# Kernel optimization log

Hardware: AMD Instinct MI355X
Metric: run time of the kernel (lower is better)

Reference implementation:

```python
import jax, jax.numpy as jnp
import numpy as np

V, E, H, F, A, L = 32000, 256, 512, 512, 256, 49  # vocab, embed, hidden, feature, attn, n_locations
B, T = 64, 32


def setup_inputs() -> dict:
    key = jax.random.key(0)
    ks = jax.random.split(key, 16)
    s = lambda k, sh: (jax.random.normal(k, sh, jnp.float32) * 0.02)
    embedding = s(ks[0], (V, E)).at[0].set(0.0)  # padding_idx=0 row zeroed
    return dict(
        image_feats=jax.random.normal(ks[1], (B, L, F), jnp.float32),
        caption_in=jax.random.randint(ks[2], (B, T), 0, V, dtype=jnp.int32),
        embedding=embedding,
        W_init_h=s(ks[3], (F, H)), b_init_h=jnp.zeros((H,), jnp.float32),
        W_init_c=s(ks[4], (F, H)), b_init_c=jnp.zeros((H,), jnp.float32),
        W_feat=s(ks[5], (F, A)), b_feat=jnp.zeros((A,), jnp.float32),
        W_hid=s(ks[6], (H, A)), b_hid=jnp.zeros((A,), jnp.float32),
        W_score=s(ks[7], (A,)), b_score=jnp.zeros((), jnp.float32),
        W_ih=s(ks[8], (E + F, 4 * H)), b_ih=jnp.zeros((4 * H,), jnp.float32),
        W_hh=s(ks[9], (H, 4 * H)), b_hh=jnp.zeros((4 * H,), jnp.float32),
        W_out=s(ks[10], (H, V)), b_out=jnp.zeros((V,), jnp.float32),
    )


def reference(image_feats, caption_in, embedding,
              W_init_h, b_init_h, W_init_c, b_init_c,
              W_feat, b_feat, W_hid, b_hid, W_score, b_score,
              W_ih, b_ih, W_hh, b_hh, W_out, b_out):
    # init_hidden_state: mean over spatial locations -> two linears
    mean_feats = image_feats.mean(axis=1)                      # (B, F)
    h0 = mean_feats @ W_init_h + b_init_h                      # (B, H)
    c0 = mean_feats @ W_init_c + b_init_c                      # (B, H)
    embs = embedding[caption_in]                               # (B, T, E); dropout = identity (eval)
    feat_proj = image_feats @ W_feat + b_feat                  # (B, L, A) - invariant over t, precompute

    def step(carry, emb_t):
        h, c = carry
        # additive attention
        energy = jnp.tanh(feat_proj + (h @ W_hid + b_hid)[:, None, :])   # (B, L, A)
        scores = energy @ W_score + b_score                              # (B, L)
        alpha = jax.nn.softmax(scores, axis=1)                           # (B, L)
        context = jnp.einsum('bl,blf->bf', alpha, image_feats)           # (B, F)
        # LSTMCell (torch gate order i, f, g, o)
        x = jnp.concatenate([emb_t, context], axis=1)                    # (B, E+F)
        gates = x @ W_ih + b_ih + h @ W_hh + b_hh                        # (B, 4H)
        i, f, g, o = jnp.split(gates, 4, axis=1)
        i = jax.nn.sigmoid(i); f = jax.nn.sigmoid(f); o = jax.nn.sigmoid(o)
        c_new = f * c + i * jnp.tanh(g)
        h_new = o * jnp.tanh(c_new)
        logits_t = h_new @ W_out + b_out                                 # (B, V); dropout = identity
        return (h_new, c_new), (logits_t, alpha)

    _, (logits, alphas) = jax.lax.scan(step, (h0, c0), jnp.swapaxes(embs, 0, 1))
    predictions = jnp.swapaxes(logits, 0, 1)   # (B, T, V)
    all_alphas = jnp.swapaxes(alphas, 0, 1)    # (B, T, L)
    return predictions, all_alphas
```

## Files before the change

kernel.cpp:

```cpp
#include <hip/hip_runtime.h>
#include <hip/hip_bf16.h>

typedef _Float16 f16;
typedef _Float16 f16x8 __attribute__((ext_vector_type(8)));
typedef _Float16 f16x4 __attribute__((ext_vector_type(4)));
typedef _Float16 f16x2 __attribute__((ext_vector_type(2)));
typedef float f32x4 __attribute__((ext_vector_type(4)));
typedef unsigned long long ull;

#define B_ 64
#define T_ 32
#define L_ 49
#define F_ 512
#define H_ 512
#define A_ 256
#define E_ 256
#define V_ 32000
#define G4 2048
#define NG 32
#define NLOG 125
#define SLOT 16

#define ALOAD32(p)     __hip_atomic_load((const unsigned*)(p), __ATOMIC_RELAXED, __HIP_MEMORY_SCOPE_AGENT)
#define ASTORE32(p, v) __hip_atomic_store((unsigned*)(p), (v), __ATOMIC_RELAXED, __HIP_MEMORY_SCOPE_AGENT)
#define ASTORE64(p, v) __hip_atomic_store((ull*)(p), (v), __ATOMIC_RELAXED, __HIP_MEMORY_SCOPE_AGENT)

#if defined(__has_builtin)
#if __has_builtin(__builtin_amdgcn_fdot2)
#define HAS_FDOT2 1
#endif
#endif

#define NB_TC0 (64 * 24)
#define NB_TC1 (64 * 16)
#define NB_TC2 (1000 * 16)
#define NB_TC3 (8 * 16)
#define NB_CVT 1568
#define NB_EMB 2048
#define NB_INIT 64
#define NB_FP  196

__device__ void dev_tcvt(const float* __restrict__ x, f16* __restrict__ y,
                         int R, int C, int bx, int by, char* smem) {
    float (*ls)[33] = (float(*)[33])smem;
    int c0 = bx * 32, r0 = by * 32;
    int tid = threadIdx.x;
    int rr = tid >> 3, cs = (tid & 7) * 4;
    float4 v = *(const float4*)&x[(size_t)(r0 + rr) * C + c0 + cs];
    ls[rr][cs] = v.x; ls[rr][cs + 1] = v.y; ls[rr][cs + 2] = v.z; ls[rr][cs + 3] = v.w;
    __syncthreads();
    int cr = tid >> 3, rs = (tid & 7) * 4;
    f16x4 o = {(f16)ls[rs][cr], (f16)ls[rs + 1][cr], (f16)ls[rs + 2][cr], (f16)ls[rs + 3][cr]};
    *(f16x4*)&y[(size_t)(c0 + cr) * R + r0 + rs] = o;
}

__global__ __launch_bounds__(256) void k_prep(
    const float* __restrict__ image_feats, const int* __restrict__ caption,
    const float* __restrict__ embedding,
    const float* __restrict__ W_init_h, const float* __restrict__ b_init_h,
    const float* __restrict__ W_init_c, const float* __restrict__ b_init_c,
    const float* __restrict__ W_feat, const float* __restrict__ b_feat,
    const float* __restrict__ W_hid, const float* __restrict__ W_ih,
    const float* __restrict__ W_hh, const float* __restrict__ W_out,
    f16* __restrict__ feats16, f16* __restrict__ embs16,
    f16* __restrict__ WihT, f16* __restrict__ WhhT,
    f16* __restrict__ WoutT, f16* __restrict__ WhidT,
    f16* __restrict__ hslab, float* __restrict__ c_cur,
    float* __restrict__ featproj) {
    __shared__ __align__(16) char smem[32768];
    int bid = blockIdx.x, tid = threadIdx.x;
    int r = bid;
    if (r < NB_TC0) { dev_tcvt(W_ih, WihT, E_ + F_, G4, r % 64, r / 64, smem); return; }
    r -= NB_TC0;
    if (r < NB_TC1) { dev_tcvt(W_hh, WhhT, H_, G4, r % 64, r / 64, smem); return; }
    r -= NB_TC1;
    if (r < NB_TC2) { dev_tcvt(W_out, WoutT, H_, V_, r % 1000, r / 1000, smem); return; }
    r -= NB_TC2;
    if (r < NB_TC3) { dev_tcvt(W_hid, WhidT, H_, A_, r % 8, r / 8, smem); return; }
    r -= NB_TC3;
    if (r < NB_CVT) {
        int i = r * 256 + tid;
        float4 v = ((const float4*)image_feats)[i];
        f16x4 h = {(f16)v.x, (f16)v.y, (f16)v.z, (f16)v.w};
        ((f16x4*)feats16)[i] = h;
        return;
    }
    r -= NB_CVT;
    if (r < NB_EMB) {
        int tok = caption[r];
        embs16[(size_t)r * E_ + tid] = (f16)embedding[(size_t)tok * E_ + tid];
        return;
    }
    r -= NB_EMB;
    if (r < NB_INIT) {
        float* mean = (float*)smem;
        int b = r;
        for (int f = tid; f < F_; f += 256) {
            float s = 0.f;
            for (int l = 0; l < L_; ++l) s += image_feats[((size_t)b * L_ + l) * F_ + f];
            mean[f] = s * (1.f / 49.f);
        }
        __syncthreads();
        for (int h = tid; h < H_; h += 256) {
            float a = b_init_h[h], c = b_init_c[h];
            for (int k = 0; k < F_; ++k) {
                float m = mean[k];
                a += m * W_init_h[k * H_ + h];
                c += m * W_init_c[k * H_ + h];
            }
            hslab[(size_t)b * H_ + h] = (f16)a;
            c_cur[b * H_ + h] = c;
        }
        return;
    }
    r -= NB_INIT;
    {
        float (*fs)[F_] = (float(*)[F_])smem;
        int r0 = r * 16;
        for (int i = tid; i < 16 * F_; i += 256)
            fs[i >> 9][i & 511] = image_feats[(size_t)r0 * F_ + i];
        __syncthreads();
        float acc[16];
#pragma unroll
        for (int q = 0; q < 16; ++q) acc[q] = 0.f;
        for (int k = 0; k < F_; ++k) {
            float w = W_feat[k * A_ + tid];
#pragma unroll
            for (int q = 0; q < 16; ++q) acc[q] += fs[q][k] * w;
        }
        float bb = b_feat[tid];
#pragma unroll
        for (int q = 0; q < 16; ++q) featproj[(size_t)(r0 + q) * A_ + tid] = acc[q] + bb;
    }
}

struct Smem128 { f16 As[128][40]; f16 Bs[128][40]; };

__device__ __forceinline__ void gemm128_body1(
    const f16* __restrict__ A, int lda, const f16* __restrict__ Bt, int ldb,
    f16* __restrict__ Cv, int M, int K, int mtiles, int bid,
    const float* __restrict__ bias0, const float* __restrict__ bias1, Smem128* sm) {
    int m0 = (bid % mtiles) * 128, n0 = (bid / mtiles) * 128;
    int tid = threadIdx.x, lane = tid & 63, wave = tid >> 6;
    int wr = (wave >> 1) * 64, wc = (wave & 1) * 64;
    int frow = lane & 15, fk = (lane >> 4) * 8;
    int ra = tid >> 2, ka = (tid & 3) * 8;
    f32x4 acc[4][4];
#pragma unroll
    for (int i = 0; i < 4; ++i)
#pragma unroll
        for (int j = 0; j < 4; ++j) { acc[i][j][0]=0.f; acc[i][j][1]=0.f; acc[i][j][2]=0.f; acc[i][j][3]=0.f; }

    for (int k0 = 0; k0 < K; k0 += 32) {
        f16x8 a0 = *(const f16x8*)&A[(size_t)(m0 + ra) * lda + k0 + ka];
        f16x8 a1 = *(const f16x8*)&A[(size_t)(m0 + 64 + ra) * lda + k0 + ka];
        f16x8 b0 = *(const f16x8*)&Bt[(size_t)(n0 + ra) * ldb + k0 + ka];
        f16x8 b1 = *(const f16x8*)&Bt[(size_t)(n0 + 64 + ra) * ldb + k0 + ka];
        __syncthreads();
        *(f16x8*)&sm->As[ra][ka] = a0;
        *(f16x8*)&sm->As[64 + ra][ka] = a1;
        *(f16x8*)&sm->Bs[ra][ka] = b0;
        *(f16x8*)&sm->Bs[64 + ra][ka] = b1;
        __syncthreads();
        f16x8 av[4], bv[4];
#pragma unroll
        for (int i = 0; i < 4; ++i) {
            av[i] = *(f16x8*)&sm->As[wr + i * 16 + frow][fk];
            bv[i] = *(f16x8*)&sm->Bs[wc + i * 16 + frow][fk];
        }
#pragma unroll
        for (int mi = 0; mi < 4; ++mi)
#pragma unroll
            for (int ni = 0; ni < 4; ++ni)
                acc[mi][ni] = __builtin_amdgcn_mfma_f32_16x16x32_f16(av[mi], bv[ni], acc[mi][ni], 0, 0, 0);
    }
    int rq = (lane >> 4) * 4;
#pragma unroll
    for (int mi = 0; mi < 4; ++mi)
#pragma unroll
        for (int ni = 0; ni < 4; ++ni) {
            int cc = n0 + wc + ni * 16 + frow;
            float badd = (bias0 ? bias0[cc] : 0.f) + (bias1 ? bias1[cc] : 0.f);
#pragma unroll
            for (int r = 0; r < 4; ++r) {
                int rr = m0 + wr + mi * 16 + rq + r;
                if (rr < M)
                    Cv[((size_t)rr * 512 + (cc & 511)) * 4 + (cc >> 9)] =
                        (f16)(acc[mi][ni][r] + badd);
            }
        }
}

__global__ __launch_bounds__(256) void k_gemm_pre(
    int split,
    const f16* A0, int lda0, const f16* B0, int ldb0, f16* C0, int M0, int K0, int mt0,
    const f16* A1, int lda1, const f16* B1, int ldb1, f16* C1, int M1, int K1, int mt1,
    const float* bias0, const float* bias1) {
    __shared__ Smem128 sm;
    int bid = blockIdx.x;
    if (bid < split)
        gemm128_body1(A0, lda0, B0, ldb0, C0, M0, K0, mt0, bid,
                      (const float*)nullptr, (const float*)nullptr, &sm);
    else
        gemm128_body1(A1, lda1, B1, ldb1, C1, M1, K1, mt1, bid - split,
                      bias0, bias1, &sm);
}

struct GateSm {
    float fp[L_][A_];
    float ea[A_];
    float ws[A_];
    float sc[64];
    float alpha[64];
    unsigned hL[256];
};
struct GemmSm {
    f16 w[64][512];
    union {
        f16 hs[64][512];
        f16 hwT16[64][72];
    } u;
};
struct LogSm { f16 hs[128][512]; };

__device__ __forceinline__ void wait_n(const unsigned* flags, int n, unsigned target) {
    int tid = threadIdx.x;
    if (tid < n) {
        const unsigned* p = flags + tid * SLOT;
        while (ALOAD32(p) < target) __builtin_amdgcn_s_sleep(1);
    }
    asm volatile("" ::: "memory");
    __syncthreads();
}

__device__ __forceinline__ float sigm(float x) { return 1.f / (1.f + __expf(-x)); }
__device__ __forceinline__ float tanh_f(float x) { return 1.f - 2.f / (1.f + __expf(2.f * x)); }

__global__ __launch_bounds__(256, 1) void k_steps(
    const f16* __restrict__ WhhT, const f16* __restrict__ WhidT,
    const float* __restrict__ featproj, const float* __restrict__ b_hid,
    const float* __restrict__ W_score, const float* __restrict__ b_score,
    const f16* __restrict__ embP, const f16* __restrict__ fp2P,
    const float* __restrict__ c_cur,
    f16* __restrict__ hslab, f16* __restrict__ hwslab,
    const f16* __restrict__ WoutT, const float* __restrict__ b_out,
    float* __restrict__ preds, float* __restrict__ out_alpha,
    unsigned* __restrict__ gateflag, unsigned* __restrict__ gemmflag) {
    __shared__ __align__(16) char smraw[sizeof(LogSm)];
    int bid = blockIdx.x, tid = threadIdx.x;

    if (bid < 64) {
        int b = bid;
        GateSm* S = (GateSm*)smraw;
        for (int i = tid; i < L_ * A_; i += 256)
            ((float*)S->fp)[i] = featproj[(size_t)b * L_ * A_ + i];
        S->ws[tid] = W_score[tid];
        float bhid_r = b_hid[tid];
        float bsc = b_score[0];
        S->hL[tid] = ((const unsigned*)hslab)[(size_t)b * 256 + tid];
        float cs0 = c_cur[b * H_ + 2 * tid], cs1 = c_cur[b * H_ + 2 * tid + 1];
        const f16* wrow = WhidT + (size_t)tid * 512;
        int wv = tid >> 6, ln = tid & 63;
        __syncthreads();

        for (int t = 0; t < T_; ++t) {
            {
                float acc = bhid_r;
                const f16x8* hL8 = (const f16x8*)S->hL;
#pragma unroll 16
                for (int kk = 0; kk < 64; ++kk) {
                    union { f16x8 v; f16x2 p[4]; } uw, uh;
                    uw.v = *(const f16x8*)&wrow[kk * 8];
                    uh.v = hL8[kk];
#ifdef HAS_FDOT2
                    acc = __builtin_amdgcn_fdot2(uw.p[0], uh.p[0], acc, false);
                    acc = __builtin_amdgcn_fdot2(uw.p[1], uh.p[1], acc, false);
                    acc = __builtin_amdgcn_fdot2(uw.p[2], uh.p[2], acc, false);
                    acc = __builtin_amdgcn_fdot2(uw.p[3], uh.p[3], acc, false);
#else
#pragma unroll
                    for (int e = 0; e < 8; ++e) acc += (float)uw.v[e] * (float)uh.v[e];
#endif
                }
                S->ea[tid] = acc;
            }
            __syncthreads();
            for (int l = wv; l < L_; l += 4) {
                float p = 0.f;
#pragma unroll
                for (int q = 0; q < 4; ++q) {
                    int j = ln + q * 64;
                    p += tanh_f(S->fp[l][j] + S->ea[j]) * S->ws[j];
                }
#pragma unroll
                for (int off = 32; off > 0; off >>= 1) p += __shfl_xor(p, off);
                if (ln == 0) S->sc[l] = p;
            }
            __syncthreads();
            if (tid < 64) {
                float v = (tid < L_) ? S->sc[tid] + bsc : -3.4e38f;
                float m = v;
#pragma unroll
                for (int off = 32; off > 0; off >>= 1) m = fmaxf(m, __shfl_xor(m, off));
                float e = (tid < L_) ? __expf(v - m) : 0.f;
                float s = e;
#pragma unroll
                for (int off = 32; off > 0; off >>= 1) s += __shfl_xor(s, off);
                if (tid < L_) {
                    float al = e / s;
                    S->alpha[tid] = al;
                    out_alpha[((size_t)b * T_ + t) * L_ + tid] = al;
                }
            }
            __syncthreads();
            float s8[8];
#pragma unroll
            for (int i = 0; i < 8; ++i) s8[i] = 0.f;
            {
                const f16* fpb = fp2P + (size_t)b * L_ * G4 + 8 * tid;
#pragma unroll 7
                for (int l = 0; l < L_; ++l) {
                    float a = S->alpha[l];
                    f16x8 fv = *(const f16x8*)&fpb[(size_t)l * G4];
#pragma unroll
                    for (int i = 0; i < 8; ++i) s8[i] += a * (float)fv[i];
                }
            }
            f16x8 ep = *(const f16x8*)&embP[((size_t)b * T_ + t) * G4 + 8 * tid];
            wait_n(gemmflag, NG, (unsigned)(t + 1));
            {
                f16x8 hw = *(const f16x8*)&hwslab[((size_t)t * B_ + b) * G4 + 8 * tid];
                float gA[8];
#pragma unroll
                for (int i = 0; i < 8; ++i) gA[i] = (float)hw[i] + (float)ep[i] + s8[i];
                float cn0 = sigm(gA[1]) * cs0 + sigm(gA[0]) * tanh_f(gA[2]);
                float cn1 = sigm(gA[5]) * cs1 + sigm(gA[4]) * tanh_f(gA[6]);
                float hn0 = sigm(gA[3]) * tanh_f(cn0);
                float hn1 = sigm(gA[7]) * tanh_f(cn1);
                cs0 = cn0; cs1 = cn1;
                union { f16 h[2]; unsigned u; } pk;
                pk.h[0] = (f16)hn0; pk.h[1] = (f16)hn1;
                S->hL[tid] = pk.u;
                ASTORE32((unsigned*)hslab + ((size_t)(t + 1) * B_ + b) * 256 + tid, pk.u);
            }
            __syncthreads();
            if (tid == 0)
                ASTORE32(&gateflag[b * SLOT], (unsigned)(t + 2));
        }
    } else if (bid < 64 + NG) {
        int g = bid - 64;
        GemmSm* S = (GemmSm*)smraw;
        for (int i = 0; i < 16; ++i) {
            int idx = i * 256 + tid;
            int r = idx >> 6, ch = idx & 63;
            int cc = (r & 3) * 512 + 16 * g + (r >> 2);
            *(f16x8*)&S->w[r][(ch ^ (r & 7)) * 8] =
                *(const f16x8*)&WhhT[(size_t)cc * 512 + ch * 8];
        }
        int wvv = tid >> 6, lane = tid & 63;
        int frow = lane & 15, q = lane >> 4, sw = frow & 7, rq = q * 4;
        int bo = tid >> 2, cq = (tid & 3) * 4;
        __syncthreads();

        for (int t = 0; t < T_; ++t) {
            if (t) wait_n(gateflag, 64, (unsigned)(t + 1));
            {
                const f16* hsrc = hslab + (size_t)t * B_ * H_;
#pragma unroll
                for (int i = 0; i < 16; ++i) {
                    int idx = i * 256 + tid;
                    int r = idx >> 6, ch = idx & 63;
                    *(f16x8*)&S->u.hs[r][(ch ^ (r & 7)) * 8] =
                        *(const f16x8*)&hsrc[(size_t)r * H_ + ch * 8];
                }
            }
            __syncthreads();
            f32x4 a4[4];
#pragma unroll
            for (int mi = 0; mi < 4; ++mi) { a4[mi][0]=0.f; a4[mi][1]=0.f; a4[mi][2]=0.f; a4[mi][3]=0.f; }
#pragma unroll
            for (int kk = 0; kk < 16; ++kk) {
                int ch = ((kk * 4 + q) ^ sw) * 8;
                f16x8 bv = *(f16x8*)&S->w[wvv * 16 + frow][ch];
#pragma unroll
                for (int mi = 0; mi < 4; ++mi) {
                    f16x8 av = *(f16x8*)&S->u.hs[mi * 16 + frow][ch];
                    a4[mi] = __builtin_amdgcn_mfma_f32_16x16x32_f16(av, bv, a4[mi], 0, 0, 0);
                }
            }
            __syncthreads();
#pragma unroll
            for (int mi = 0; mi < 4; ++mi)
#pragma unroll
                for (int r = 0; r < 4; ++r)
                    S->u.hwT16[mi * 16 + rq + r][wvv * 16 + frow] = (f16)a4[mi][r];
            __syncthreads();
            {
                f16* dst = hwslab + ((size_t)t * B_ + bo) * G4 + 64 * g + cq;
#pragma unroll
                for (int e = 0; e < 4; ++e) {
                    union { f16 h[4]; ull u; } pk;
                    *(f16x4*)pk.h = *(f16x4*)&S->u.hwT16[bo][cq + 16 * e];
                    ASTORE64(dst + 16 * e, pk.u);
                }
            }
            __syncthreads();
            if (tid == 0)
                ASTORE32(&gemmflag[g * SLOT], (unsigned)(t + 1));
        }
    } else {
        int nt = bid - 64 - NG;
        int n0 = nt * 256;
        LogSm* S = (LogSm*)smraw;
        int wvv = tid >> 6, lane = tid & 63;
        int frow = lane & 15, q = lane >> 4, sw = frow & 7, rq = q * 4;

        for (int tc = 0; tc < T_ / 2; ++tc) {
            wait_n(gateflag, 64, (unsigned)(2 * tc + 3));
            {
                const f16* hsrc = hslab + (size_t)(2 * tc + 1) * B_ * H_;
#pragma unroll
                for (int i = 0; i < 32; ++i) {
                    int idx = i * 256 + tid;
                    int r = idx >> 6, ch = idx & 63;
                    *(f16x8*)&S->hs[r][(ch ^ (r & 7)) * 8] =
                        *(const f16x8*)&hsrc[(size_t)r * H_ + ch * 8];
                }
            }
            __syncthreads();
            f32x4 acc[8][4];
#pragma unroll
            for (int mi = 0; mi < 8; ++mi)
#pragma unroll
                for (int ni = 0; ni < 4; ++ni) { acc[mi][ni][0]=0.f; acc[mi][ni][1]=0.f; acc[mi][ni][2]=0.f; acc[mi][ni][3]=0.f; }
#pragma unroll 2
            for (int kk = 0; kk < 16; ++kk) {
                int ch = ((kk * 4 + q) ^ sw) * 8;
                f16x8 av[8], bv[4];
#pragma unroll
                for (int mi = 0; mi < 8; ++mi)
                    av[mi] = *(f16x8*)&S->hs[mi * 16 + frow][ch];
#pragma unroll
                for (int ni = 0; ni < 4; ++ni)
                    bv[ni] = *(const f16x8*)&WoutT[(size_t)(n0 + wvv * 64 + ni * 16 + frow) * 512 + kk * 32 + q * 8];
#pragma unroll
                for (int mi = 0; mi < 8; ++mi)
#pragma unroll
                    for (int ni = 0; ni < 4; ++ni)
                        acc[mi][ni] = __builtin_amdgcn_mfma_f32_16x16x32_f16(av[mi], bv[ni], acc[mi][ni], 0, 0, 0);
            }
#pragma unroll
            for (int ni = 0; ni < 4; ++ni) {
                int cc = n0 + wvv * 64 + ni * 16 + frow;
                float badd = b_out[cc];
#pragma unroll
                for (int mi = 0; mi < 8; ++mi)
#pragma unroll
                    for (int r = 0; r < 4; ++r) {
                        int rr = mi * 16 + rq + r;
                        int tt = 2 * tc + (rr >> 6), bb2 = rr & 63;
                        preds[((size_t)bb2 * T_ + tt) * V_ + cc] = acc[mi][ni][r] + badd;
                    }
            }
            __syncthreads();
        }
    }
}

extern "C" void kernel_launch(void* const* d_in, const int* in_sizes, int n_in,
                              void* d_out, int out_size, void* d_ws, size_t ws_size,
                              hipStream_t stream) {
    const float* image_feats = (const float*)d_in[0];
    const int*   caption     = (const int*)d_in[1];
    const float* embedding   = (const float*)d_in[2];
    const float* W_init_h    = (const float*)d_in[3];
    const float* b_init_h    = (const float*)d_in[4];
    const float* W_init_c    = (const float*)d_in[5];
    const float* b_init_c    = (const float*)d_in[6];
    const float* W_feat      = (const float*)d_in[7];
    const float* b_feat      = (const float*)d_in[8];
    const float* W_hid       = (const float*)d_in[9];
    const float* b_hid       = (const float*)d_in[10];
    const float* W_score     = (const float*)d_in[11];
    const float* b_score     = (const float*)d_in[12];
    const float* W_ih        = (const float*)d_in[13];
    const float* b_ih        = (const float*)d_in[14];
    const float* W_hh        = (const float*)d_in[15];
    const float* b_hh        = (const float*)d_in[16];
    const float* W_out       = (const float*)d_in[17];
    const float* b_out       = (const float*)d_in[18];

    float* preds = (float*)d_out;
    float* out_alpha = preds + (size_t)B_ * T_ * V_;

    size_t off = 0;
    char* base = (char*)d_ws;
    auto carve = [&](size_t bytes) {
        void* p = base + off;
        off += (bytes + 255) & ~(size_t)255;
        return p;
    };
    const int MP = 3200;
    f16* fp2P       = (f16*)carve((size_t)MP * G4 * 2);
    f16* embP       = (f16*)carve((size_t)B_ * T_ * G4 * 2);
    float* featproj = (float*)carve((size_t)B_ * L_ * A_ * 4);
    float* c_cur    = (float*)carve((size_t)B_ * H_ * 4);
    f16* hslab      = (f16*)carve((size_t)(T_ + 1) * B_ * H_ * 2);
    f16* hwslab     = (f16*)carve((size_t)T_ * B_ * G4 * 2);
    unsigned* flags = (unsigned*)carve((64 + NG) * SLOT * 4);
    f16* feats16    = (f16*)carve((size_t)MP * F_ * 2);
    f16* embs16     = (f16*)carve((size_t)B_ * T_ * E_ * 2);
    f16* WihT       = (f16*)carve((size_t)G4 * (E_ + F_) * 2);
    f16* WhhT       = (f16*)carve((size_t)G4 * H_ * 2);
    f16* WoutT      = (f16*)carve((size_t)V_ * H_ * 2);
    f16* WhidT      = (f16*)carve((size_t)A_ * H_ * 2);
    unsigned* gateflag = flags;
    unsigned* gemmflag = flags + 64 * SLOT;
    (void)ws_size; (void)in_sizes; (void)n_in; (void)out_size;

    {
        int nb = NB_TC0 + NB_TC1 + NB_TC2 + NB_TC3 + NB_CVT + NB_EMB + NB_INIT + NB_FP;
        hipLaunchKernelGGL(k_prep, dim3(nb), dim3(256), 0, stream,
                           image_feats, caption, embedding,
                           W_init_h, b_init_h, W_init_c, b_init_c,
                           W_feat, b_feat, W_hid, W_ih, W_hh, W_out,
                           feats16, embs16, WihT, WhhT, WoutT, WhidT,
                           hslab, c_cur, featproj);
    }
    hipLaunchKernelGGL(k_gemm_pre, dim3(400 + 256), dim3(256), 0, stream,
                       400,
                       feats16, F_, WihT + E_, E_ + F_, fp2P, B_ * L_, F_, 25,
                       embs16, E_, WihT, E_ + F_, embP, B_ * T_, E_, B_ * T_ / 128,
                       b_ih, b_hh);
    hipMemsetAsync(flags, 0, (64 + NG) * SLOT * 4, stream);
    hipLaunchKernelGGL(k_steps, dim3(64 + NG + NLOG), dim3(256), 0, stream,
                       WhhT, WhidT, featproj, b_hid, W_score, b_score,
                       embP, fp2P, c_cur, hslab, hwslab,
                       WoutT, b_out, preds, out_alpha,
                       gateflag, gemmflag);
}
```

Baseline: 728.9 us.

## Compute context in-loop and fuse context-weight GEMM into recurrent gate GEMM

Stops precomputing the feats@W_ih_ctx projection for all 3136 locations (fp2P). Instead each gate block computes the attention context vector from LDS-resident fp16 feats and publishes it with a new ctx flag. The GEMM blocks, now doubled to 64 with half the columns each, add context@W_ih_ctx to h@W_hh. W_hid is also repacked into k-pair interleaved form for coalesced fdot2 reads. This removes a large pre-GEMM and the per-step fp2P reads, at the cost of an extra synchronization hop and a second GEMM inside the serial recurrent critical path.

```diff
diff --git a/kernel.cpp b/kernel.cpp
--- a/kernel.cpp
+++ b/kernel.cpp
@@ -17,7 +17,7 @@
 #define E_ 256
 #define V_ 32000
 #define G4 2048
-#define NG 32
+#define NG 64
 #define NLOG 125
 #define SLOT 16
 
@@ -34,7 +34,7 @@
 #define NB_TC0 (64 * 24)
 #define NB_TC1 (64 * 16)
 #define NB_TC2 (1000 * 16)
-#define NB_TC3 (8 * 16)
+#define NB_PAIR 256
 #define NB_CVT 1568
 #define NB_EMB 2048
 #define NB_INIT 64
@@ -64,7 +64,7 @@
     const float* __restrict__ W_hh, const float* __restrict__ W_out,
     f16* __restrict__ feats16, f16* __restrict__ embs16,
     f16* __restrict__ WihT, f16* __restrict__ WhhT,
-    f16* __restrict__ WoutT, f16* __restrict__ WhidT,
+    f16* __restrict__ WoutT, f16* __restrict__ Whidp,
     f16* __restrict__ hslab, float* __restrict__ c_cur,
     float* __restrict__ featproj) {
     __shared__ __align__(16) char smem[32768];
@@ -76,8 +76,13 @@
     r -= NB_TC1;
     if (r < NB_TC2) { dev_tcvt(W_out, WoutT, H_, V_, r % 1000, r / 1000, smem); return; }
     r -= NB_TC2;
-    if (r < NB_TC3) { dev_tcvt(W_hid, WhidT, H_, A_, r % 8, r / 8, smem); return; }
-    r -= NB_TC3;
+    if (r < NB_PAIR) {
+        int k2 = r;
+        Whidp[(k2 * 256 + tid) * 2]     = (f16)W_hid[(2 * k2) * 256 + tid];
+        Whidp[(k2 * 256 + tid) * 2 + 1] = (f16)W_hid[(2 * k2 + 1) * 256 + tid];
+        return;
+    }
+    r -= NB_PAIR;
     if (r < NB_CVT) {
         int i = r * 256 + tid;
         float4 v = ((const float4*)image_feats)[i];
@@ -136,10 +141,12 @@
 
 struct Smem128 { f16 As[128][40]; f16 Bs[128][40]; };
 
-__device__ __forceinline__ void gemm128_body1(
-    const f16* __restrict__ A, int lda, const f16* __restrict__ Bt, int ldb,
-    f16* __restrict__ Cv, int M, int K, int mtiles, int bid,
-    const float* __restrict__ bias0, const float* __restrict__ bias1, Smem128* sm) {
+__global__ __launch_bounds__(256) void k_gemm_emb(
+    const f16* __restrict__ A, const f16* __restrict__ Bt,
+    f16* __restrict__ Cv, const float* __restrict__ bias0, const float* __restrict__ bias1) {
+    __shared__ Smem128 sm;
+    int bid = blockIdx.x;
+    int mtiles = B_ * T_ / 128;
     int m0 = (bid % mtiles) * 128, n0 = (bid / mtiles) * 128;
     int tid = threadIdx.x, lane = tid & 63, wave = tid >> 6;
     int wr = (wave >> 1) * 64, wc = (wave & 1) * 64;
@@ -150,23 +157,22 @@
     for (int i = 0; i < 4; ++i)
 #pragma unroll
         for (int j = 0; j < 4; ++j) { acc[i][j][0]=0.f; acc[i][j][1]=0.f; acc[i][j][2]=0.f; acc[i][j][3]=0.f; }
-
-    for (int k0 = 0; k0 < K; k0 += 32) {
-        f16x8 a0 = *(const f16x8*)&A[(size_t)(m0 + ra) * lda + k0 + ka];
-        f16x8 a1 = *(const f16x8*)&A[(size_t)(m0 + 64 + ra) * lda + k0 + ka];
-        f16x8 b0 = *(const f16x8*)&Bt[(size_t)(n0 + ra) * ldb + k0 + ka];
-        f16x8 b1 = *(const f16x8*)&Bt[(size_t)(n0 + 64 + ra) * ldb + k0 + ka];
+    for (int k0 = 0; k0 < E_; k0 += 32) {
+        f16x8 a0 = *(const f16x8*)&A[(size_t)(m0 + ra) * E_ + k0 + ka];
+        f16x8 a1 = *(const f16x8*)&A[(size_t)(m0 + 64 + ra) * E_ + k0 + ka];
+        f16x8 b0 = *(const f16x8*)&Bt[(size_t)(n0 + ra) * (E_ + F_) + k0 + ka];
+        f16x8 b1 = *(const f16x8*)&Bt[(size_t)(n0 + 64 + ra) * (E_ + F_) + k0 + ka];
         __syncthreads();
-        *(f16x8*)&sm->As[ra][ka] = a0;
-        *(f16x8*)&sm->As[64 + ra][ka] = a1;
-        *(f16x8*)&sm->Bs[ra][ka] = b0;
-        *(f16x8*)&sm->Bs[64 + ra][ka] = b1;
+        *(f16x8*)&sm.As[ra][ka] = a0;
+        *(f16x8*)&sm.As[64 + ra][ka] = a1;
+        *(f16x8*)&sm.Bs[ra][ka] = b0;
+        *(f16x8*)&sm.Bs[64 + ra][ka] = b1;
         __syncthreads();
         f16x8 av[4], bv[4];
 #pragma unroll
         for (int i = 0; i < 4; ++i) {
-            av[i] = *(f16x8*)&sm->As[wr + i * 16 + frow][fk];
-            bv[i] = *(f16x8*)&sm->Bs[wc + i * 16 + frow][fk];
+            av[i] = *(f16x8*)&sm.As[wr + i * 16 + frow][fk];
+            bv[i] = *(f16x8*)&sm.Bs[wc + i * 16 + frow][fk];
         }
 #pragma unroll
         for (int mi = 0; mi < 4; ++mi)
@@ -180,34 +186,19 @@
 #pragma unroll
         for (int ni = 0; ni < 4; ++ni) {
             int cc = n0 + wc + ni * 16 + frow;
-            float badd = (bias0 ? bias0[cc] : 0.f) + (bias1 ? bias1[cc] : 0.f);
+            float badd = bias0[cc] + bias1[cc];
 #pragma unroll
             for (int r = 0; r < 4; ++r) {
                 int rr = m0 + wr + mi * 16 + rq + r;
-                if (rr < M)
-                    Cv[((size_t)rr * 512 + (cc & 511)) * 4 + (cc >> 9)] =
-                        (f16)(acc[mi][ni][r] + badd);
-            }
-        }
-}
-
-__global__ __launch_bounds__(256) void k_gemm_pre(
-    int split,
-    const f16* A0, int lda0, const f16* B0, int ldb0, f16* C0, int M0, int K0, int mt0,
-    const f16* A1, int lda1, const f16* B1, int ldb1, f16* C1, int M1, int K1, int mt1,
-    const float* bias0, const float* bias1) {
-    __shared__ Smem128 sm;
-    int bid = blockIdx.x;
-    if (bid < split)
-        gemm128_body1(A0, lda0, B0, ldb0, C0, M0, K0, mt0, bid,
-                      (const float*)nullptr, (const float*)nullptr, &sm);
-    else
-        gemm128_body1(A1, lda1, B1, ldb1, C1, M1, K1, mt1, bid - split,
-                      bias0, bias1, &sm);
+                Cv[((size_t)rr * 512 + (cc & 511)) * 4 + (cc >> 9)] =
+                    (f16)(acc[mi][ni][r] + badd);
+            }
+        }
 }
 
 struct GateSm {
     float fp[L_][A_];
+    unsigned fe[L_ * 256];
     float ea[A_];
     float ws[A_];
     float sc[64];
@@ -215,10 +206,11 @@
     unsigned hL[256];
 };
 struct GemmSm {
-    f16 w[64][512];
+    f16 w[32][512];
+    f16 w2[32][512];
     union {
         f16 hs[64][512];
-        f16 hwT16[64][72];
+        f16 hwT16[64][40];
     } u;
 };
 struct LogSm { f16 hs[128][512]; };
@@ -237,15 +229,17 @@
 __device__ __forceinline__ float tanh_f(float x) { return 1.f - 2.f / (1.f + __expf(2.f * x)); }
 
 __global__ __launch_bounds__(256, 1) void k_steps(
-    const f16* __restrict__ WhhT, const f16* __restrict__ WhidT,
-    const float* __restrict__ featproj, const float* __restrict__ b_hid,
+    const f16* __restrict__ WhhT, const f16* __restrict__ WihT,
+    const f16* __restrict__ Whidp,
+    const float* __restrict__ featproj, const f16* __restrict__ feats16,
+    const float* __restrict__ b_hid,
     const float* __restrict__ W_score, const float* __restrict__ b_score,
-    const f16* __restrict__ embP, const f16* __restrict__ fp2P,
-    const float* __restrict__ c_cur,
-    f16* __restrict__ hslab, f16* __restrict__ hwslab,
+    const f16* __restrict__ embP, const float* __restrict__ c_cur,
+    f16* __restrict__ hslab, f16* __restrict__ ctxslab, f16* __restrict__ hwcslab,
     const f16* __restrict__ WoutT, const float* __restrict__ b_out,
     float* __restrict__ preds, float* __restrict__ out_alpha,
-    unsigned* __restrict__ gateflag, unsigned* __restrict__ gemmflag) {
+    unsigned* __restrict__ gateflag, unsigned* __restrict__ ctxflag,
+    unsigned* __restrict__ gemmflag) {
     __shared__ __align__(16) char smraw[sizeof(LogSm)];
     int bid = blockIdx.x, tid = threadIdx.x;
 
@@ -254,32 +248,32 @@
         GateSm* S = (GateSm*)smraw;
         for (int i = tid; i < L_ * A_; i += 256)
             ((float*)S->fp)[i] = featproj[(size_t)b * L_ * A_ + i];
+        {
+            const f16x8* src = (const f16x8*)(feats16 + (size_t)b * L_ * F_);
+            f16x8* dst = (f16x8*)S->fe;
+            for (int i = tid; i < L_ * F_ / 8; i += 256) dst[i] = src[i];
+        }
         S->ws[tid] = W_score[tid];
         float bhid_r = b_hid[tid];
         float bsc = b_score[0];
         S->hL[tid] = ((const unsigned*)hslab)[(size_t)b * 256 + tid];
         float cs0 = c_cur[b * H_ + 2 * tid], cs1 = c_cur[b * H_ + 2 * tid + 1];
-        const f16* wrow = WhidT + (size_t)tid * 512;
+        const unsigned* wp32 = (const unsigned*)Whidp;
         int wv = tid >> 6, ln = tid & 63;
         __syncthreads();
 
         for (int t = 0; t < T_; ++t) {
             {
                 float acc = bhid_r;
-                const f16x8* hL8 = (const f16x8*)S->hL;
 #pragma unroll 16
-                for (int kk = 0; kk < 64; ++kk) {
-                    union { f16x8 v; f16x2 p[4]; } uw, uh;
-                    uw.v = *(const f16x8*)&wrow[kk * 8];
-                    uh.v = hL8[kk];
+                for (int k2 = 0; k2 < 256; ++k2) {
+                    union { unsigned u; f16x2 v; } w, h;
+                    w.u = wp32[k2 * 256 + tid];
+                    h.u = S->hL[k2];
 #ifdef HAS_FDOT2
-                    acc = __builtin_amdgcn_fdot2(uw.p[0], uh.p[0], acc, false);
-                    acc = __builtin_amdgcn_fdot2(uw.p[1], uh.p[1], acc, false);
-                    acc = __builtin_amdgcn_fdot2(uw.p[2], uh.p[2], acc, false);
-                    acc = __builtin_amdgcn_fdot2(uw.p[3], uh.p[3], acc, false);
+                    acc = __builtin_amdgcn_fdot2(w.v, h.v, acc, false);
 #else
-#pragma unroll
-                    for (int e = 0; e < 8; ++e) acc += (float)uw.v[e] * (float)uh.v[e];
+                    acc += (float)w.v.x * (float)h.v.x + (float)w.v.y * (float)h.v.y;
 #endif
                 }
                 S->ea[tid] = acc;
@@ -313,26 +307,29 @@
                 }
             }
             __syncthreads();
-            float s8[8];
-#pragma unroll
-            for (int i = 0; i < 8; ++i) s8[i] = 0.f;
-            {
-                const f16* fpb = fp2P + (size_t)b * L_ * G4 + 8 * tid;
+            {
+                float c0 = 0.f, c1 = 0.f;
 #pragma unroll 7
                 for (int l = 0; l < L_; ++l) {
                     float a = S->alpha[l];
-                    f16x8 fv = *(const f16x8*)&fpb[(size_t)l * G4];
-#pragma unroll
-                    for (int i = 0; i < 8; ++i) s8[i] += a * (float)fv[i];
-                }
-            }
+                    union { unsigned u; f16x2 v; } fv;
+                    fv.u = S->fe[l * 256 + tid];
+                    c0 += a * (float)fv.v.x;
+                    c1 += a * (float)fv.v.y;
+                }
+                union { f16 h[2]; unsigned u; } pk;
+                pk.h[0] = (f16)c0; pk.h[1] = (f16)c1;
+                ASTORE32((unsigned*)ctxslab + ((size_t)t * B_ + b) * 256 + tid, pk.u);
+            }
+            __syncthreads();
+            if (tid == 0) ASTORE32(&ctxflag[b * SLOT], (unsigned)(t + 1));
             f16x8 ep = *(const f16x8*)&embP[((size_t)b * T_ + t) * G4 + 8 * tid];
             wait_n(gemmflag, NG, (unsigned)(t + 1));
             {
-                f16x8 hw = *(const f16x8*)&hwslab[((size_t)t * B_ + b) * G4 + 8 * tid];
+                f16x8 hw = *(const f16x8*)&hwcslab[((size_t)t * B_ + b) * G4 + 8 * tid];
                 float gA[8];
 #pragma unroll
-                for (int i = 0; i < 8; ++i) gA[i] = (float)hw[i] + (float)ep[i] + s8[i];
+                for (int i = 0; i < 8; ++i) gA[i] = (float)hw[i] + (float)ep[i];
                 float cn0 = sigm(gA[1]) * cs0 + sigm(gA[0]) * tanh_f(gA[2]);
                 float cn1 = sigm(gA[5]) * cs1 + sigm(gA[4]) * tanh_f(gA[6]);
                 float hn0 = sigm(gA[3]) * tanh_f(cn0);
@@ -350,16 +347,19 @@
     } else if (bid < 64 + NG) {
         int g = bid - 64;
         GemmSm* S = (GemmSm*)smraw;
-        for (int i = 0; i < 16; ++i) {
+        for (int i = 0; i < 8; ++i) {
             int idx = i * 256 + tid;
             int r = idx >> 6, ch = idx & 63;
-            int cc = (r & 3) * 512 + 16 * g + (r >> 2);
+            int cc = (r & 3) * 512 + 8 * g + (r >> 2);
             *(f16x8*)&S->w[r][(ch ^ (r & 7)) * 8] =
                 *(const f16x8*)&WhhT[(size_t)cc * 512 + ch * 8];
+            *(f16x8*)&S->w2[r][(ch ^ (r & 7)) * 8] =
+                *(const f16x8*)&WihT[(size_t)cc * (E_ + F_) + E_ + ch * 8];
         }
         int wvv = tid >> 6, lane = tid & 63;
         int frow = lane & 15, q = lane >> 4, sw = frow & 7, rq = q * 4;
-        int bo = tid >> 2, cq = (tid & 3) * 4;
+        int mb = (wvv >> 1) * 32, c16 = (wvv & 1) * 16;
+        int bo = tid >> 2, cq = (tid & 3) * 8;
         __syncthreads();
 
         for (int t = 0; t < T_; ++t) {
@@ -375,34 +375,53 @@
                 }
             }
             __syncthreads();
-            f32x4 a4[4];
-#pragma unroll
-            for (int mi = 0; mi < 4; ++mi) { a4[mi][0]=0.f; a4[mi][1]=0.f; a4[mi][2]=0.f; a4[mi][3]=0.f; }
+            f32x4 a4[2];
+            a4[0][0]=0.f; a4[0][1]=0.f; a4[0][2]=0.f; a4[0][3]=0.f;
+            a4[1][0]=0.f; a4[1][1]=0.f; a4[1][2]=0.f; a4[1][3]=0.f;
 #pragma unroll
             for (int kk = 0; kk < 16; ++kk) {
                 int ch = ((kk * 4 + q) ^ sw) * 8;
-                f16x8 bv = *(f16x8*)&S->w[wvv * 16 + frow][ch];
-#pragma unroll
-                for (int mi = 0; mi < 4; ++mi) {
-                    f16x8 av = *(f16x8*)&S->u.hs[mi * 16 + frow][ch];
-                    a4[mi] = __builtin_amdgcn_mfma_f32_16x16x32_f16(av, bv, a4[mi], 0, 0, 0);
-                }
-            }
-            __syncthreads();
-#pragma unroll
-            for (int mi = 0; mi < 4; ++mi)
+                f16x8 bv = *(f16x8*)&S->w[c16 + frow][ch];
+                f16x8 av0 = *(f16x8*)&S->u.hs[mb + frow][ch];
+                f16x8 av1 = *(f16x8*)&S->u.hs[mb + 16 + frow][ch];
+                a4[0] = __builtin_amdgcn_mfma_f32_16x16x32_f16(av0, bv, a4[0], 0, 0, 0);
+                a4[1] = __builtin_amdgcn_mfma_f32_16x16x32_f16(av1, bv, a4[1], 0, 0, 0);
+            }
+            wait_n(ctxflag, 64, (unsigned)(t + 1));
+            {
+                const f16* csrc = ctxslab + (size_t)t * B_ * F_;
+#pragma unroll
+                for (int i = 0; i < 16; ++i) {
+                    int idx = i * 256 + tid;
+                    int r = idx >> 6, ch = idx & 63;
+                    *(f16x8*)&S->u.hs[r][(ch ^ (r & 7)) * 8] =
+                        *(const f16x8*)&csrc[(size_t)r * F_ + ch * 8];
+                }
+            }
+            __syncthreads();
+#pragma unroll
+            for (int kk = 0; kk < 16; ++kk) {
+                int ch = ((kk * 4 + q) ^ sw) * 8;
+                f16x8 bv = *(f16x8*)&S->w2[c16 + frow][ch];
+                f16x8 av0 = *(f16x8*)&S->u.hs[mb + frow][ch];
+                f16x8 av1 = *(f16x8*)&S->u.hs[mb + 16 + frow][ch];
+                a4[0] = __builtin_amdgcn_mfma_f32_16x16x32_f16(av0, bv, a4[0], 0, 0, 0);
+                a4[1] = __builtin_amdgcn_mfma_f32_16x16x32_f16(av1, bv, a4[1], 0, 0, 0);
+            }
+            __syncthreads();
+#pragma unroll
+            for (int mi = 0; mi < 2; ++mi)
 #pragma unroll
                 for (int r = 0; r < 4; ++r)
-                    S->u.hwT16[mi * 16 + rq + r][wvv * 16 + frow] = (f16)a4[mi][r];
-            __syncthreads();
-            {
-                f16* dst = hwslab + ((size_t)t * B_ + bo) * G4 + 64 * g + cq;
-#pragma unroll
-                for (int e = 0; e < 4; ++e) {
-                    union { f16 h[4]; ull u; } pk;
-                    *(f16x4*)pk.h = *(f16x4*)&S->u.hwT16[bo][cq + 16 * e];
-                    ASTORE64(dst + 16 * e, pk.u);
-                }
+                    S->u.hwT16[mb + mi * 16 + rq + r][c16 + frow] = (f16)a4[mi][r];
+            __syncthreads();
+            {
+                f16* dst = hwcslab + ((size_t)t * B_ + bo) * G4 + 32 * g + cq;
+                union { f16 h[4]; ull u; } pk0, pk1;
+                *(f16x4*)pk0.h = *(f16x4*)&S->u.hwT16[bo][cq];
+                *(f16x4*)pk1.h = *(f16x4*)&S->u.hwT16[bo][cq + 4];
+                ASTORE64(dst, pk0.u);
+                ASTORE64(dst + 4, pk1.u);
             }
             __syncthreads();
             if (tid == 0)
@@ -500,42 +519,40 @@
         off += (bytes + 255) & ~(size_t)255;
         return p;
     };
-    const int MP = 3200;
-    f16* fp2P       = (f16*)carve((size_t)MP * G4 * 2);
     f16* embP       = (f16*)carve((size_t)B_ * T_ * G4 * 2);
     float* featproj = (float*)carve((size_t)B_ * L_ * A_ * 4);
     float* c_cur    = (float*)carve((size_t)B_ * H_ * 4);
     f16* hslab      = (f16*)carve((size_t)(T_ + 1) * B_ * H_ * 2);
-    f16* hwslab     = (f16*)carve((size_t)T_ * B_ * G4 * 2);
-    unsigned* flags = (unsigned*)carve((64 + NG) * SLOT * 4);
-    f16* feats16    = (f16*)carve((size_t)MP * F_ * 2);
+    f16* ctxslab    = (f16*)carve((size_t)T_ * B_ * F_ * 2);
+    f16* hwcslab    = (f16*)carve((size_t)T_ * B_ * G4 * 2);
+    unsigned* flags = (unsigned*)carve((64 + 64 + NG) * SLOT * 4);
+    f16* feats16    = (f16*)carve((size_t)B_ * L_ * F_ * 2);
     f16* embs16     = (f16*)carve((size_t)B_ * T_ * E_ * 2);
     f16* WihT       = (f16*)carve((size_t)G4 * (E_ + F_) * 2);
     f16* WhhT       = (f16*)carve((size_t)G4 * H_ * 2);
     f16* WoutT      = (f16*)carve((size_t)V_ * H_ * 2);
-    f16* WhidT      = (f16*)carve((size_t)A_ * H_ * 2);
+    f16* Whidp      = (f16*)carve((size_t)H_ * A_ * 2);
     unsigned* gateflag = flags;
-    unsigned* gemmflag = flags + 64 * SLOT;
+    unsigned* ctxflag  = flags + 64 * SLOT;
+    unsigned* gemmflag = flags + 128 * SLOT;
     (void)ws_size; (void)in_sizes; (void)n_in; (void)out_size;
 
     {
-        int nb = NB_TC0 + NB_TC1 + NB_TC2 + NB_TC3 + NB_CVT + NB_EMB + NB_INIT + NB_FP;
+        int nb = NB_TC0 + NB_TC1 + NB_TC2 + NB_PAIR + NB_CVT + NB_EMB + NB_INIT + NB_FP;
         hipLaunchKernelGGL(k_prep, dim3(nb), dim3(256), 0, stream,
                            image_feats, caption, embedding,
                            W_init_h, b_init_h, W_init_c, b_init_c,
                            W_feat, b_feat, W_hid, W_ih, W_hh, W_out,
-                           feats16, embs16, WihT, WhhT, WoutT, WhidT,
+                           feats16, embs16, WihT, WhhT, WoutT, Whidp,
                            hslab, c_cur, featproj);
     }
-    hipLaunchKernelGGL(k_gemm_pre, dim3(400 + 256), dim3(256), 0, stream,
-                       400,
-                       feats16, F_, WihT + E_, E_ + F_, fp2P, B_ * L_, F_, 25,
-                       embs16, E_, WihT, E_ + F_, embP, B_ * T_, E_, B_ * T_ / 128,
-                       b_ih, b_hh);
-    hipMemsetAsync(flags, 0, (64 + NG) * SLOT * 4, stream);
+    hipLaunchKernelGGL(k_gemm_emb, dim3((B_ * T_ / 128) * (G4 / 128)), dim3(256), 0, stream,
+                       embs16, WihT, embP, b_ih, b_hh);
+    hipMemsetAsync(flags, 0, (64 + 64 + NG) * SLOT * 4, stream);
     hipLaunchKernelGGL(k_steps, dim3(64 + NG + NLOG), dim3(256), 0, stream,
-                       WhhT, WhidT, featproj, b_hid, W_score, b_score,
-                       embP, fp2P, c_cur, hslab, hwslab,
+                       WhhT, WihT, Whidp, featproj, feats16, b_hid,
+                       W_score, b_score, embP, c_cur,
+                       hslab, ctxslab, hwcslab,
                        WoutT, b_out, preds, out_alpha,
-                       gateflag, gemmflag);
+                       gateflag, ctxflag, gemmflag);
 }
```

Measured after the change: 668.9 us. -8.2%, faster.
